# Kernel optimization log

Measured on AMD Instinct MI355X. Metric: run time of the kernel, lower is better.

## Reference

```python
import jax, jax.numpy as jnp
import numpy as np

B, D, NSEQ = 8, 512, 32
L0 = NSEQ * NSEQ          # 1024
H, DH = 8, 64             # n_head, d_head; H*DH == D
DFF = 2048
NLAYER = 2
EPS = 1e-6
SCALE = 1.0 / (DH ** 0.5)


def setup_inputs() -> dict:
    key = jax.random.key(0)
    ks = jax.random.split(key, 16)
    s = lambda fan: 1.0 / np.sqrt(fan)
    return {
        "embed1": jax.random.normal(ks[0], (B, D, L0), jnp.float32),
        "embed2": jax.random.normal(ks[1], (B, D, L0), jnp.float32),
        "cls_token": jax.random.normal(ks[2], (1, 1, D), jnp.float32),
        "Wq": jax.random.normal(ks[3], (NLAYER, D, D), jnp.float32) * s(D),
        "bq": jnp.zeros((NLAYER, D), jnp.float32),
        "Wk": jax.random.normal(ks[4], (NLAYER, D, D), jnp.float32) * s(D),
        "bk": jnp.zeros((NLAYER, D), jnp.float32),
        "Wv": jax.random.normal(ks[5], (NLAYER, D, D), jnp.float32) * s(D),
        "bv": jnp.zeros((NLAYER, D), jnp.float32),
        "Wo": jax.random.normal(ks[6], (NLAYER, D, D), jnp.float32) * s(D),
        "bo": jnp.zeros((NLAYER, D), jnp.float32),
        "ln1_g": jnp.ones((NLAYER, D), jnp.float32),
        "ln1_b": jnp.zeros((NLAYER, D), jnp.float32),
        "W1": jax.random.normal(ks[7], (NLAYER, DFF, D), jnp.float32) * s(D),
        "b1": jnp.zeros((NLAYER, DFF), jnp.float32),
        "W2": jax.random.normal(ks[8], (NLAYER, D, DFF), jnp.float32) * s(DFF),
        "b2": jnp.zeros((NLAYER, D), jnp.float32),
        "ln2_g": jnp.ones((NLAYER, D), jnp.float32),
        "ln2_b": jnp.zeros((NLAYER, D), jnp.float32),
    }


def _ln(x, g, b):
    m = jnp.mean(x, axis=-1, keepdims=True)
    v = jnp.mean(jnp.square(x - m), axis=-1, keepdims=True)
    return (x - m) * jax.lax.rsqrt(v + EPS) * g + b


def reference(embed1, embed2, cls_token, Wq, bq, Wk, bk, Wv, bv, Wo, bo,
              ln1_g, ln1_b, W1, b1, W2, b2, ln2_g, ln2_b):
    b = embed1.shape[0]
    cls = jnp.broadcast_to(cls_token, (b, 1, D))
    # [B, L0, D] with prepended cls -> [B, L, D]
    x1 = jnp.concatenate([cls, jnp.transpose(embed1, (0, 2, 1))], axis=1)
    x2 = jnp.concatenate([cls, jnp.transpose(embed2, (0, 2, 1))], axis=1)
    # mask_inputs is all ones vs i_pad=0 -> attn_mask all False (no masking)
    x = x1
    for l in range(NLAYER):
        q = (x  @ Wq[l].T + bq[l]).reshape(b, -1, H, DH)   # [B,L,H,DH]
        k = (x2 @ Wk[l].T + bk[l]).reshape(b, -1, H, DH)
        v = (x2 @ Wv[l].T + bv[l]).reshape(b, -1, H, DH)
        scores = jnp.einsum('bqhd,bkhd->bhqk', q, k) * SCALE
        attn = jax.nn.softmax(scores, axis=-1)
        ctx = jnp.einsum('bhqk,bkhd->bqhd', attn, v).reshape(b, -1, H * DH)
        att_out = ctx @ Wo[l].T + bo[l]
        x = _ln(x + att_out, ln1_g[l], ln1_b[l])
        h = jax.nn.gelu(x @ W1[l].T + b1[l], approximate=False)
        ffn = h @ W2[l].T + b2[l]
        x = _ln(x + ffn, ln2_g[l], ln2_b[l])
    return x
```

## Files before the change

kernel.cpp:

```cpp
#include <hip/hip_runtime.h>
#include <hip/hip_bf16.h>

constexpr int B_   = 8;
constexpr int D_   = 512;
constexpr int L0_  = 1024;
constexpr int L_   = 1025;
constexpr int H_   = 8;
constexpr int DH_  = 64;
constexpr int DFF_ = 2048;
constexpr int NLAYER_ = 2;
constexpr int M_   = B_ * L_;
constexpr int LP_  = 1088;
constexpr int NQT_ = 9;
constexpr int NSPLIT_ = 2;
constexpr float EPS_   = 1e-6f;
constexpr float SCALE_ = 0.125f;

#define DEV_INLINE __device__ __forceinline__

typedef __attribute__((ext_vector_type(8))) __bf16 bf16x8;
typedef __attribute__((ext_vector_type(4))) __bf16 bf16x4;
typedef __attribute__((ext_vector_type(4))) float  f32x4;
typedef __attribute__((ext_vector_type(4))) unsigned int u32x4;

union U4 { uint32_t u[4]; bf16x8 f; };

DEV_INLINE float gelu_exact(float x) {
    return 0.5f * x * (1.f + erff(x * 0.70710678118654752f));
}

DEV_INLINE uint16_t bfbits(float v) {
    __bf16 h = (__bf16)v;
    return __builtin_bit_cast(uint16_t, h);
}
DEV_INLINE uint32_t pk2f(float a, float b) {
    return (uint32_t)bfbits(a) | ((uint32_t)bfbits(b) << 16);
}
DEV_INLINE float bf2f(uint32_t bits16) {
    uint32_t u = bits16 << 16;
    return __builtin_bit_cast(float, u);
}

__global__ __launch_bounds__(256) void tobf16_kernel(
    const float* __restrict__ src, __bf16* __restrict__ dst, int n4) {
    int i = blockIdx.x * 256 + threadIdx.x;
    if (i >= n4) return;
    float4 v = *(const float4*)&src[i * 4];
    bf16x4 h;
    h[0] = (__bf16)v.x; h[1] = (__bf16)v.y;
    h[2] = (__bf16)v.z; h[3] = (__bf16)v.w;
    *(bf16x4*)&dst[i * 4] = h;
}

__global__ __launch_bounds__(256) void zero_vt_pad_kernel(__bf16* __restrict__ Vt) {
    constexpr int PAD = LP_ - L_;
    int idx = blockIdx.x * 256 + threadIdx.x;
    int total = B_ * H_ * DH_ * PAD;
    if (idx >= total) return;
    int row = idx / PAD;
    int c   = idx - row * PAD;
    Vt[(size_t)row * LP_ + L_ + c] = (__bf16)0.f;
}

__global__ __launch_bounds__(256) void write_cls_kernel(
    const float* __restrict__ cls, float* __restrict__ X1, float* __restrict__ X2) {
    int idx = blockIdx.x * 256 + threadIdx.x;
    int b = idx >> 9;
    int d = idx & 511;
    float v = cls[d];
    X1[(size_t)b * L_ * D_ + d] = v;
    X2[(size_t)b * L_ * D_ + d] = v;
}

__global__ __launch_bounds__(256) void transpose_embed_kernel(
    const float* __restrict__ e, float* __restrict__ X) {
    __shared__ float tile[32][33];
    int b  = blockIdx.z;
    int i0 = blockIdx.x * 32;
    int d0 = blockIdx.y * 32;
    int tx = threadIdx.x;
    int ty = threadIdx.y;
#pragma unroll
    for (int j = 0; j < 32; j += 8)
        tile[ty + j][tx] = e[((size_t)b * D_ + d0 + ty + j) * L0_ + i0 + tx];
    __syncthreads();
#pragma unroll
    for (int j = 0; j < 32; j += 8)
        X[((size_t)b * L_ + 1 + i0 + ty + j) * D_ + d0 + tx] = tile[tx][ty + j];
}

template <bool GELU, int OUTMODE>
__global__ __launch_bounds__(256) void gemm_mfma_kernel(
    const __bf16* __restrict__ A, const __bf16* __restrict__ Wh,
    const float* __restrict__ bias, float* __restrict__ C,
    __bf16* __restrict__ Ch, int M, int N, int K, float oscale) {
    constexpr int BM = 128, BN = 64, BK = 64;
    constexpr int LDK = BK + 8;
    __shared__ alignas(16) __bf16 Ahs[BM][LDK];
    __shared__ alignas(16) __bf16 Bhs[BN][LDK];

    const int GM = (M + BM - 1) / BM;
    const int nwg = gridDim.x;
    int bid = blockIdx.x;
    {
        int q = nwg >> 3, r = nwg & 7;
        int xcd = bid & 7, pos = bid >> 3;
        bid = (xcd < r) ? xcd * (q + 1) + pos
                        : r * (q + 1) + (xcd - r) * q + pos;
    }
    const int bn = bid / GM;
    const int bm = bid % GM;
    const int m0 = bm * BM;
    const int n0 = bn * BN;

    const int tid  = threadIdx.x;
    const int lane = tid & 63;
    const int wv   = tid >> 6;
    const int wr   = wv >> 1;
    const int wc   = wv & 1;
    const int fr   = lane & 15;
    const int fq   = lane >> 4;
    const int fq8  = fq * 8;
    const int mb   = wr * 64;
    const int nb   = wc * 32;

    const int srow = tid >> 2;
    const int scol = (tid & 3) * 16;
    size_t aOff[2];
#pragma unroll
    for (int rep = 0; rep < 2; ++rep) {
        int r = m0 + srow + rep * 64;
        if (r > M - 1) r = M - 1;
        aOff[rep] = (size_t)r * K + scol;
    }
    const size_t wOff = (size_t)(n0 + srow) * K + scol;

    f32x4 acc[4][2];
#pragma unroll
    for (int i = 0; i < 4; ++i)
#pragma unroll
        for (int j = 0; j < 2; ++j) acc[i][j] = (f32x4){0.f, 0.f, 0.f, 0.f};

    const int nk = K / BK;
    u32x4 aR[2][2], wR[2];
#pragma unroll
    for (int rep = 0; rep < 2; ++rep) {
        aR[rep][0] = *(const u32x4*)&A[aOff[rep]];
        aR[rep][1] = *(const u32x4*)&A[aOff[rep] + 8];
    }
    wR[0] = *(const u32x4*)&Wh[wOff];
    wR[1] = *(const u32x4*)&Wh[wOff + 8];

    for (int kt = 0; kt < nk; ++kt) {
#pragma unroll
        for (int rep = 0; rep < 2; ++rep) {
            *(u32x4*)&Ahs[srow + rep * 64][scol]     = aR[rep][0];
            *(u32x4*)&Ahs[srow + rep * 64][scol + 8] = aR[rep][1];
        }
        *(u32x4*)&Bhs[srow][scol]     = wR[0];
        *(u32x4*)&Bhs[srow][scol + 8] = wR[1];
        __syncthreads();

        if (kt + 1 < nk) {
            int k0 = (kt + 1) * BK;
#pragma unroll
            for (int rep = 0; rep < 2; ++rep) {
                aR[rep][0] = *(const u32x4*)&A[aOff[rep] + k0];
                aR[rep][1] = *(const u32x4*)&A[aOff[rep] + k0 + 8];
            }
            wR[0] = *(const u32x4*)&Wh[wOff + k0];
            wR[1] = *(const u32x4*)&Wh[wOff + k0 + 8];
        }

#pragma unroll
        for (int ks = 0; ks < 2; ++ks) {
            bf16x8 ah[4], bh[2];
#pragma unroll
            for (int i = 0; i < 4; ++i)
                ah[i] = *(bf16x8*)&Ahs[mb + i * 16 + fr][ks * 32 + fq8];
#pragma unroll
            for (int j = 0; j < 2; ++j)
                bh[j] = *(bf16x8*)&Bhs[nb + j * 16 + fr][ks * 32 + fq8];
#pragma unroll
            for (int i = 0; i < 4; ++i)
#pragma unroll
                for (int j = 0; j < 2; ++j)
                    acc[i][j] = __builtin_amdgcn_mfma_f32_16x16x32_bf16(ah[i], bh[j], acc[i][j], 0, 0, 0);
        }
        __syncthreads();
    }

    const int ccol0 = n0 + nb + fr;
    const float b0 = bias[ccol0];
    const float b1 = bias[ccol0 + 16];
#pragma unroll
    for (int i = 0; i < 4; ++i) {
#pragma unroll
        for (int r = 0; r < 4; ++r) {
            int row = m0 + mb + i * 16 + fq * 4 + r;
            if (row < M) {
                float v0 = acc[i][0][r] + b0;
                float v1 = acc[i][1][r] + b1;
                if (GELU) { v0 = gelu_exact(v0); v1 = gelu_exact(v1); }
                v0 *= oscale;
                v1 *= oscale;
                if (OUTMODE == 2) {
                    Ch[(size_t)row * N + ccol0]      = (__bf16)v0;
                    Ch[(size_t)row * N + ccol0 + 16] = (__bf16)v1;
                } else {
                    C[(size_t)row * N + ccol0]      = v0;
                    C[(size_t)row * N + ccol0 + 16] = v1;
                }
            }
        }
    }
}

__global__ __launch_bounds__(256) void gemm_kv_kernel(
    const __bf16* __restrict__ A, const __bf16* __restrict__ Wh,
    const float* __restrict__ biasK, const float* __restrict__ biasV,
    __bf16* __restrict__ Kb, __bf16* __restrict__ Vt) {
    constexpr int BM = 128, BN = 64, BK = 64, K = 512;
    constexpr int LDK = BK + 8;
    __shared__ alignas(16) __bf16 Ahs[BM][LDK];
    __shared__ alignas(16) __bf16 Bhs[BN][LDK];

    const int GM = (M_ + BM - 1) / BM;
    const int nwg = gridDim.x;
    int bid = blockIdx.x;
    {
        int q = nwg >> 3, r = nwg & 7;
        int xcd = bid & 7, pos = bid >> 3;
        bid = (xcd < r) ? xcd * (q + 1) + pos
                        : r * (q + 1) + (xcd - r) * q + pos;
    }
    const int bn = bid / GM;
    const int bm = bid % GM;
    const int m0 = bm * BM;
    const int n0 = bn * BN;

    const int tid  = threadIdx.x;
    const int lane = tid & 63;
    const int wv   = tid >> 6;
    const int wr   = wv >> 1;
    const int wc   = wv & 1;
    const int fr   = lane & 15;
    const int fq   = lane >> 4;
    const int fq8  = fq * 8;
    const int mb   = wr * 64;
    const int nb   = wc * 32;

    const int srow = tid >> 2;
    const int scol = (tid & 3) * 16;
    size_t aOff[2];
#pragma unroll
    for (int rep = 0; rep < 2; ++rep) {
        int r = m0 + srow + rep * 64;
        if (r > M_ - 1) r = M_ - 1;
        aOff[rep] = (size_t)r * K + scol;
    }
    const size_t wOff = (size_t)(n0 + srow) * K + scol;

    f32x4 acc[4][2];
#pragma unroll
    for (int i = 0; i < 4; ++i)
#pragma unroll
        for (int j = 0; j < 2; ++j) acc[i][j] = (f32x4){0.f, 0.f, 0.f, 0.f};

    const int nk = K / BK;
    u32x4 aR[2][2], wR[2];
#pragma unroll
    for (int rep = 0; rep < 2; ++rep) {
        aR[rep][0] = *(const u32x4*)&A[aOff[rep]];
        aR[rep][1] = *(const u32x4*)&A[aOff[rep] + 8];
    }
    wR[0] = *(const u32x4*)&Wh[wOff];
    wR[1] = *(const u32x4*)&Wh[wOff + 8];

    for (int kt = 0; kt < nk; ++kt) {
#pragma unroll
        for (int rep = 0; rep < 2; ++rep) {
            *(u32x4*)&Ahs[srow + rep * 64][scol]     = aR[rep][0];
            *(u32x4*)&Ahs[srow + rep * 64][scol + 8] = aR[rep][1];
        }
        *(u32x4*)&Bhs[srow][scol]     = wR[0];
        *(u32x4*)&Bhs[srow][scol + 8] = wR[1];
        __syncthreads();

        if (kt + 1 < nk) {
            int k0 = (kt + 1) * BK;
#pragma unroll
            for (int rep = 0; rep < 2; ++rep) {
                aR[rep][0] = *(const u32x4*)&A[aOff[rep] + k0];
                aR[rep][1] = *(const u32x4*)&A[aOff[rep] + k0 + 8];
            }
            wR[0] = *(const u32x4*)&Wh[wOff + k0];
            wR[1] = *(const u32x4*)&Wh[wOff + k0 + 8];
        }

#pragma unroll
        for (int ks = 0; ks < 2; ++ks) {
            bf16x8 ah[4], bh[2];
#pragma unroll
            for (int i = 0; i < 4; ++i)
                ah[i] = *(bf16x8*)&Ahs[mb + i * 16 + fr][ks * 32 + fq8];
#pragma unroll
            for (int j = 0; j < 2; ++j)
                bh[j] = *(bf16x8*)&Bhs[nb + j * 16 + fr][ks * 32 + fq8];
#pragma unroll
            for (int i = 0; i < 4; ++i)
#pragma unroll
                for (int j = 0; j < 2; ++j)
                    acc[i][j] = __builtin_amdgcn_mfma_f32_16x16x32_bf16(ah[i], bh[j], acc[i][j], 0, 0, 0);
        }
        __syncthreads();
    }

    const int ccol0 = n0 + nb + fr;
    if (n0 < 512) {
        const float b0 = biasK[ccol0];
        const float b1 = biasK[ccol0 + 16];
#pragma unroll
        for (int i = 0; i < 4; ++i) {
#pragma unroll
            for (int r = 0; r < 4; ++r) {
                int row = m0 + mb + i * 16 + fq * 4 + r;
                if (row < M_) {
                    Kb[(size_t)row * 512 + ccol0]      = (__bf16)(acc[i][0][r] + b0);
                    Kb[(size_t)row * 512 + ccol0 + 16] = (__bf16)(acc[i][1][r] + b1);
                }
            }
        }
    } else {
        const int cv = ccol0 - 512;
        const int h2 = cv >> 6, d2 = cv & 63;
        const float b0 = biasV[cv];
        const float b1 = biasV[cv + 16];
#pragma unroll
        for (int i = 0; i < 4; ++i) {
#pragma unroll
            for (int r = 0; r < 4; ++r) {
                int row = m0 + mb + i * 16 + fq * 4 + r;
                if (row < M_) {
                    int b2 = row / L_;
                    int l2 = row - b2 * L_;
                    size_t vb = (size_t)(b2 * H_ + h2) * DH_ * LP_;
                    Vt[vb + (size_t)d2 * LP_ + l2]        = (__bf16)(acc[i][0][r] + b0);
                    Vt[vb + (size_t)(d2 + 16) * LP_ + l2] = (__bf16)(acc[i][1][r] + b1);
                }
            }
        }
    }
}

__global__ __launch_bounds__(256) void attn_mfma_kernel(
    const __bf16* __restrict__ Qb, const __bf16* __restrict__ Kb,
    const __bf16* __restrict__ Vtb, __bf16* __restrict__ Opart,
    float* __restrict__ ml) {
    constexpr int LDP = 72;
    constexpr int NT = (L_ + 63) / 64;
    __shared__ alignas(16) __bf16 Kls[64][LDP];
    __shared__ alignas(16) __bf16 Vls[64][LDP];

    const int tid  = threadIdx.x;
    const int lane = tid & 63;
    const int wv   = tid >> 6;
    const int fr   = lane & 15;
    const int fq   = lane >> 4;
    const int fq8  = fq * 8;

    int bid = blockIdx.x;
    int swz = (bid & 7) * (NSPLIT_ * NQT_ * H_ * B_ / 8) + (bid >> 3);
    const int s   = swz / (NQT_ * H_ * B_);
    int rem = swz - s * (NQT_ * H_ * B_);
    const int qt = rem % NQT_;
    const int bh = rem / NQT_;
    const int h = bh & 7, b = bh >> 3;
    const int q0 = qt * 128 + wv * 32;
    const int T0 = (NT * s) / NSPLIT_;
    const int T1 = (NT * (s + 1)) / NSPLIT_;
    const size_t obase = (size_t)b * L_ * D_ + h * DH_;

    bf16x8 bqh[2][2];
#pragma unroll
    for (int g = 0; g < 2; ++g) {
        int gq = q0 + 16 * g + fr; if (gq > L_ - 1) gq = L_ - 1;
        const __bf16* qrow = Qb + (size_t)(b * L_ + gq) * D_ + h * DH_;
#pragma unroll
        for (int ss = 0; ss < 2; ++ss)
            bqh[g][ss] = *(const bf16x8*)&qrow[ss * 32 + fq8];
    }

    float m[2] = {-1e30f, -1e30f};
    float lsum[2] = {0.f, 0.f};
    f32x4 oA[2][4];
#pragma unroll
    for (int g = 0; g < 2; ++g)
#pragma unroll
        for (int c = 0; c < 4; ++c) oA[g][c] = (f32x4){0.f, 0.f, 0.f, 0.f};

    const int sr  = tid >> 2;
    const int scb = (tid & 3) * 8;
    const size_t kRowBase = (size_t)(b * L_) * D_ + h * DH_ + scb;
    const size_t vRowBase = ((size_t)bh * DH_ + sr) * LP_ + scb;

    u32x4 kR[2], vR[2];
    {
        int gr = T0 * 64 + sr; if (gr > L_ - 1) gr = L_ - 1;
        const __bf16* kp = Kb + kRowBase + (size_t)gr * D_;
        const __bf16* vp = Vtb + vRowBase + T0 * 64;
        kR[0] = *(const u32x4*)&kp[0];  kR[1] = *(const u32x4*)&kp[32];
        vR[0] = *(const u32x4*)&vp[0];  vR[1] = *(const u32x4*)&vp[32];
        *(u32x4*)&Kls[sr][scb]      = kR[0];
        *(u32x4*)&Kls[sr][scb + 32] = kR[1];
        *(u32x4*)&Vls[sr][scb]      = vR[0];
        *(u32x4*)&Vls[sr][scb + 32] = vR[1];
    }

    for (int t = T0; t < T1; ++t) {
        const int kt = t * 64;
        __syncthreads();

        if (t + 1 < T1) {
            int gr = kt + 64 + sr; if (gr > L_ - 1) gr = L_ - 1;
            const __bf16* kp = Kb + kRowBase + (size_t)gr * D_;
            const __bf16* vp = Vtb + vRowBase + (kt + 64);
            kR[0] = *(const u32x4*)&kp[0];  kR[1] = *(const u32x4*)&kp[32];
            vR[0] = *(const u32x4*)&vp[0];  vR[1] = *(const u32x4*)&vp[32];
        }

        const bool fullTile = (kt + 64 <= L_);
        float p0[4][4], p1[4][4];
#pragma unroll
        for (int c = 0; c < 4; ++c) {
            const int row = 16 * c + fr;
            bf16x8 ah0 = *(bf16x8*)&Kls[row][fq8];
            bf16x8 ah1 = *(bf16x8*)&Kls[row][32 + fq8];
#pragma unroll
            for (int g = 0; g < 2; ++g) {
                f32x4 sacc = (f32x4){0.f, 0.f, 0.f, 0.f};
                sacc = __builtin_amdgcn_mfma_f32_16x16x32_bf16(ah0, bqh[g][0], sacc, 0, 0, 0);
                sacc = __builtin_amdgcn_mfma_f32_16x16x32_bf16(ah1, bqh[g][1], sacc, 0, 0, 0);
                if (fullTile) {
#pragma unroll
                    for (int rr = 0; rr < 4; ++rr) {
                        if (g == 0) p0[c][rr] = sacc[rr]; else p1[c][rr] = sacc[rr];
                    }
                } else {
#pragma unroll
                    for (int rr = 0; rr < 4; ++rr) {
                        int k = kt + 16 * c + 4 * fq + rr;
                        float val = (k < L_) ? sacc[rr] : -1e30f;
                        if (g == 0) p0[c][rr] = val; else p1[c][rr] = val;
                    }
                }
            }
        }

        bf16x8 pah[2][2];
#pragma unroll
        for (int g = 0; g < 2; ++g) {
            float (*p)[4] = (g == 0) ? p0 : p1;
            float t0 = p[0][0];
#pragma unroll
            for (int c = 0; c < 4; ++c)
#pragma unroll
                for (int rr = 0; rr < 4; ++rr) t0 = fmaxf(t0, p[c][rr]);
            t0 = fmaxf(t0, __shfl_xor(t0, 16));
            t0 = fmaxf(t0, __shfl_xor(t0, 32));
            float mn = fmaxf(m[g], t0);
            const bool noresc = __all(mn == m[g]);
            float sclq = noresc ? 1.f : __expf(m[g] - mn);
            m[g] = mn;
            float ls = 0.f;
#pragma unroll
            for (int c = 0; c < 4; ++c)
#pragma unroll
                for (int rr = 0; rr < 4; ++rr) {
                    float e = __expf(p[c][rr] - mn);
                    p[c][rr] = e;
                    ls += e;
                }
            ls += __shfl_xor(ls, 16);
            ls += __shfl_xor(ls, 32);
            lsum[g] = lsum[g] * sclq + ls;
            if (!noresc) {
#pragma unroll
                for (int rr = 0; rr < 4; ++rr) {
                    float sO = __shfl(sclq, 4 * fq + rr);
#pragma unroll
                    for (int c2 = 0; c2 < 4; ++c2) oA[g][c2][rr] *= sO;
                }
            }

            uint32_t pqh[4][2];
#pragma unroll
            for (int c = 0; c < 4; ++c) {
                pqh[c][0] = pk2f(p[c][0], p[c][1]);
                pqh[c][1] = pk2f(p[c][2], p[c][3]);
            }
            const int src0 = fr + ((fq & 1) << 5);
            const int src1 = src0 + 16;
            const bool sel = (fq >> 1) != 0;
#pragma unroll
            for (int ss = 0; ss < 2; ++ss) {
                const int c0 = 2 * ss, c1 = 2 * ss + 1;
                uint32_t A0 = (uint32_t)__shfl((int)pqh[c0][0], src0);
                uint32_t A1 = (uint32_t)__shfl((int)pqh[c0][1], src0);
                uint32_t A2 = (uint32_t)__shfl((int)pqh[c0][0], src1);
                uint32_t A3 = (uint32_t)__shfl((int)pqh[c0][1], src1);
                uint32_t B0 = (uint32_t)__shfl((int)pqh[c1][0], src0);
                uint32_t B1 = (uint32_t)__shfl((int)pqh[c1][1], src0);
                uint32_t B2 = (uint32_t)__shfl((int)pqh[c1][0], src1);
                uint32_t B3 = (uint32_t)__shfl((int)pqh[c1][1], src1);
                U4 uh;
                uh.u[0] = sel ? B0 : A0; uh.u[1] = sel ? B1 : A1;
                uh.u[2] = sel ? B2 : A2; uh.u[3] = sel ? B3 : A3;
                pah[g][ss] = uh.f;
            }
        }

#pragma unroll
        for (int c2 = 0; c2 < 4; ++c2) {
            const int row = 16 * c2 + fr;
            bf16x8 vh0 = *(bf16x8*)&Vls[row][fq8];
            bf16x8 vh1 = *(bf16x8*)&Vls[row][32 + fq8];
#pragma unroll
            for (int g = 0; g < 2; ++g) {
                f32x4 o = oA[g][c2];
                o = __builtin_amdgcn_mfma_f32_16x16x32_bf16(pah[g][0], vh0, o, 0, 0, 0);
                o = __builtin_amdgcn_mfma_f32_16x16x32_bf16(pah[g][1], vh1, o, 0, 0, 0);
                oA[g][c2] = o;
            }
        }

        __syncthreads();
        if (t + 1 < T1) {
            *(u32x4*)&Kls[sr][scb]      = kR[0];
            *(u32x4*)&Kls[sr][scb + 32] = kR[1];
            *(u32x4*)&Vls[sr][scb]      = vR[0];
            *(u32x4*)&Vls[sr][scb + 32] = vR[1];
        }
    }

    __bf16* Op = Opart + (size_t)s * M_ * D_;
#pragma unroll
    for (int g = 0; g < 2; ++g) {
#pragma unroll
        for (int rr = 0; rr < 4; ++rr) {
            int row = q0 + 16 * g + 4 * fq + rr;
            if (row < L_) {
#pragma unroll
                for (int c2 = 0; c2 < 4; ++c2)
                    Op[obase + (size_t)row * D_ + 16 * c2 + fr] = (__bf16)oA[g][c2][rr];
            }
        }
        if (fq == 0) {
            int qrow = q0 + 16 * g + fr;
            if (qrow < L_) {
                size_t mlidx = (((size_t)s * B_ + b) * H_ + h) * L_ + qrow;
                ml[mlidx * 2]     = m[g];
                ml[mlidx * 2 + 1] = lsum[g];
            }
        }
    }
}

__global__ __launch_bounds__(256) void attn_merge_kernel(
    const __bf16* __restrict__ Opart, const float* __restrict__ ml,
    __bf16* __restrict__ Out) {
    int idx = blockIdx.x * 256 + threadIdx.x;
    if (idx >= M_ * 64) return;
    int row = idx >> 6;
    int seg = idx & 63;
    int col0 = seg * 8;
    int h = col0 >> 6;
    int b = row / L_;
    int l = row - b * L_;
    float ms[NSPLIT_], ls[NSPLIT_];
    float mm = -1e30f;
#pragma unroll
    for (int s = 0; s < NSPLIT_; ++s) {
        size_t mi = ((((size_t)s * B_ + b) * H_ + h) * L_ + l) * 2;
        ms[s] = ml[mi];
        ls[s] = ml[mi + 1];
        mm = fmaxf(mm, ms[s]);
    }
    float wsum = 0.f, w[NSPLIT_];
#pragma unroll
    for (int s = 0; s < NSPLIT_; ++s) {
        w[s] = __expf(ms[s] - mm);
        wsum += w[s] * ls[s];
    }
    float inv = 1.f / wsum;
#pragma unroll
    for (int s = 0; s < NSPLIT_; ++s) w[s] *= inv;

    size_t base = (size_t)row * D_ + col0;
    float o[8] = {0.f, 0.f, 0.f, 0.f, 0.f, 0.f, 0.f, 0.f};
#pragma unroll
    for (int s = 0; s < NSPLIT_; ++s) {
        const __bf16* Os = Opart + (size_t)s * M_ * D_;
        u32x4 a = *(const u32x4*)&Os[base];
#pragma unroll
        for (int i = 0; i < 4; ++i) {
            o[2 * i]     += w[s] * bf2f(a[i] & 0xffffu);
            o[2 * i + 1] += w[s] * bf2f(a[i] >> 16);
        }
    }
    U4 u;
#pragma unroll
    for (int i = 0; i < 4; ++i)
        u.u[i] = pk2f(o[2 * i], o[2 * i + 1]);
    *(u32x4*)&Out[base] = *(u32x4*)&u.u[0];
}

template <bool HIOUT>
__global__ __launch_bounds__(256) void add_ln_kernel(
    const float* __restrict__ X, const float* __restrict__ Y,
    const float* __restrict__ g, const float* __restrict__ be,
    float* __restrict__ Out, __bf16* __restrict__ Oh) {
    int wave = threadIdx.x >> 6;
    int lane = threadIdx.x & 63;
    int row = blockIdx.x * 4 + wave;
    if (row >= M_) return;
    size_t base = (size_t)row * D_;
    int c0 = lane * 4, c1 = 256 + lane * 4;
    float4 xa = *(const float4*)&X[base + c0];
    float4 xb = *(const float4*)&X[base + c1];
    float4 ya = *(const float4*)&Y[base + c0];
    float4 yb = *(const float4*)&Y[base + c1];
    float v[8] = {xa.x + ya.x, xa.y + ya.y, xa.z + ya.z, xa.w + ya.w,
                  xb.x + yb.x, xb.y + yb.y, xb.z + yb.z, xb.w + yb.w};
    float s = 0.f, s2 = 0.f;
#pragma unroll
    for (int i = 0; i < 8; ++i) { s += v[i]; s2 = fmaf(v[i], v[i], s2); }
#pragma unroll
    for (int off = 32; off > 0; off >>= 1) {
        s  += __shfl_xor(s, off);
        s2 += __shfl_xor(s2, off);
    }
    float mean = s * (1.f / D_);
    float var  = s2 * (1.f / D_) - mean * mean;
    float rstd = rsqrtf(var + EPS_);
    float4 ga = *(const float4*)&g[c0];
    float4 gb = *(const float4*)&g[c1];
    float4 ba = *(const float4*)&be[c0];
    float4 bb = *(const float4*)&be[c1];
    float o[8];
    o[0] = (v[0] - mean) * rstd * ga.x + ba.x;
    o[1] = (v[1] - mean) * rstd * ga.y + ba.y;
    o[2] = (v[2] - mean) * rstd * ga.z + ba.z;
    o[3] = (v[3] - mean) * rstd * ga.w + ba.w;
    o[4] = (v[4] - mean) * rstd * gb.x + bb.x;
    o[5] = (v[5] - mean) * rstd * gb.y + bb.y;
    o[6] = (v[6] - mean) * rstd * gb.z + bb.z;
    o[7] = (v[7] - mean) * rstd * gb.w + bb.w;
    *(float4*)&Out[base + c0] = make_float4(o[0], o[1], o[2], o[3]);
    *(float4*)&Out[base + c1] = make_float4(o[4], o[5], o[6], o[7]);
    if (HIOUT) {
        bf16x4 h0, h1;
#pragma unroll
        for (int i = 0; i < 4; ++i) {
            h0[i] = (__bf16)o[i];
            h1[i] = (__bf16)o[4 + i];
        }
        *(bf16x4*)&Oh[base + c0] = h0;
        *(bf16x4*)&Oh[base + c1] = h1;
    }
}

extern "C" void kernel_launch(void* const* d_in, const int* in_sizes, int n_in,
                              void* d_out, int out_size, void* d_ws, size_t ws_size,
                              hipStream_t stream) {
    const float* embed1 = (const float*)d_in[0];
    const float* embed2 = (const float*)d_in[1];
    const float* cls    = (const float*)d_in[2];
    const float* Wq = (const float*)d_in[3];
    const float* bq = (const float*)d_in[4];
    const float* Wk = (const float*)d_in[5];
    const float* bk = (const float*)d_in[6];
    const float* Wv = (const float*)d_in[7];
    const float* bv = (const float*)d_in[8];
    const float* Wo = (const float*)d_in[9];
    const float* bo = (const float*)d_in[10];
    const float* ln1g = (const float*)d_in[11];
    const float* ln1b = (const float*)d_in[12];
    const float* W1 = (const float*)d_in[13];
    const float* b1 = (const float*)d_in[14];
    const float* W2 = (const float*)d_in[15];
    const float* b2 = (const float*)d_in[16];
    const float* ln2g = (const float*)d_in[17];
    const float* ln2b = (const float*)d_in[18];

    const size_t SZ = (size_t)M_ * D_;
    float* ws = (float*)d_ws;
    float* X   = ws;
    __bf16* Xh = (__bf16*)(ws + SZ);
    __bf16* X2h = (__bf16*)(ws + SZ + SZ / 2);
    float* Tb  = ws + 2 * SZ;
    __bf16* Tbh = (__bf16*)(ws + 2 * SZ + SZ / 2);
    __bf16* Qbh = (__bf16*)(ws + 3 * SZ);
    float* WoOut  = (float*)(ws + 3 * SZ);
    __bf16* Kbh = (__bf16*)(ws + 4 * SZ);
    __bf16* Vtb = (__bf16*)(ws + 5 * SZ);
    __bf16* Hbh = (__bf16*)(ws + 5 * SZ);
    float* mlBuf   = ws + 6 * SZ + SZ / 2;
    __bf16* Opart  = (__bf16*)(ws + 7 * SZ);
    __bf16* wreg = (__bf16*)(ws + 9 * SZ);

    const size_t NQl = (size_t)D_ * D_;
    const size_t NQ  = (size_t)NLAYER_ * NQl;
    const size_t NF  = (size_t)NLAYER_ * DFF_ * D_;
    __bf16* Wqh  = wreg;
    __bf16* Wkvh = Wqh + NQ;
    __bf16* Woh  = Wkvh + 2 * NQ;
    __bf16* W1h  = Woh + NQ;
    __bf16* W2h  = W1h + NF;

    tobf16_kernel<<<(int)(NQ / 4 + 255) / 256, 256, 0, stream>>>(Wq, Wqh, (int)(NQ / 4));
    tobf16_kernel<<<(int)(NQ / 4 + 255) / 256, 256, 0, stream>>>(Wo, Woh, (int)(NQ / 4));
    tobf16_kernel<<<(int)(NF / 4 + 255) / 256, 256, 0, stream>>>(W1, W1h, (int)(NF / 4));
    tobf16_kernel<<<(int)(NF / 4 + 255) / 256, 256, 0, stream>>>(W2, W2h, (int)(NF / 4));
    for (int l = 0; l < NLAYER_; ++l) {
        tobf16_kernel<<<(int)(NQl / 4 + 255) / 256, 256, 0, stream>>>(
            Wk + l * NQl, Wkvh + l * 2 * NQl, (int)(NQl / 4));
        tobf16_kernel<<<(int)(NQl / 4 + 255) / 256, 256, 0, stream>>>(
            Wv + l * NQl, Wkvh + l * 2 * NQl + NQl, (int)(NQl / 4));
    }

    float* X2tmp = Tb;
    write_cls_kernel<<<(B_ * D_) / 256, 256, 0, stream>>>(cls, X, X2tmp);
    transpose_embed_kernel<<<dim3(L0_ / 32, D_ / 32, B_), dim3(32, 8), 0, stream>>>(embed1, X);
    transpose_embed_kernel<<<dim3(L0_ / 32, D_ / 32, B_), dim3(32, 8), 0, stream>>>(embed2, X2tmp);
    tobf16_kernel<<<(int)(SZ / 4 + 255) / 256, 256, 0, stream>>>(X, Xh, (int)(SZ / 4));
    tobf16_kernel<<<(int)(SZ / 4 + 255) / 256, 256, 0, stream>>>(X2tmp, X2h, (int)(SZ / 4));

    const int GM = (M_ + 127) / 128;
    const int g512  = GM * (512 / 64);
    const int g1024 = GM * (1024 / 64);
    const int g2048 = GM * (2048 / 64);
    const int gpad  = (B_ * H_ * DH_ * (LP_ - L_) + 255) / 256;
    const int gmerge = (M_ * 64 + 255) / 256;

    for (int l = 0; l < NLAYER_; ++l) {
        const size_t oQ = (size_t)l * NQl;
        const size_t oF = (size_t)l * DFF_ * D_;

        gemm_mfma_kernel<false, 2><<<g512, 256, 0, stream>>>(
            Xh, Wqh + oQ, bq + l * D_, nullptr, Qbh, M_, D_, D_, SCALE_);
        gemm_kv_kernel<<<g1024, 256, 0, stream>>>(
            X2h, Wkvh + l * 2 * NQl, bk + l * D_, bv + l * D_, Kbh, Vtb);
        zero_vt_pad_kernel<<<gpad, 256, 0, stream>>>(Vtb);

        attn_mfma_kernel<<<NSPLIT_ * NQT_ * H_ * B_, 256, 0, stream>>>(
            Qbh, Kbh, Vtb, Opart, mlBuf);
        attn_merge_kernel<<<gmerge, 256, 0, stream>>>(Opart, mlBuf, Tbh);

        gemm_mfma_kernel<false, 0><<<g512, 256, 0, stream>>>(
            Tbh, Woh + oQ, bo + l * D_, WoOut, nullptr, M_, D_, D_, 1.f);

        add_ln_kernel<true><<<(M_ + 3) / 4, 256, 0, stream>>>(
            X, WoOut, ln1g + l * D_, ln1b + l * D_, X, Xh);

        gemm_mfma_kernel<true, 2><<<g2048, 256, 0, stream>>>(
            Xh, W1h + oF, b1 + l * DFF_, nullptr, Hbh, M_, DFF_, D_, 1.f);
        gemm_mfma_kernel<false, 0><<<g512, 256, 0, stream>>>(
            Hbh, W2h + oF, b2 + l * D_, Tb, nullptr, M_, D_, DFF_, 1.f);

        if (l == NLAYER_ - 1) {
            add_ln_kernel<false><<<(M_ + 3) / 4, 256, 0, stream>>>(
                X, Tb, ln2g + l * D_, ln2b + l * D_, (float*)d_out, nullptr);
        } else {
            add_ln_kernel<true><<<(M_ + 3) / 4, 256, 0, stream>>>(
                X, Tb, ln2g + l * D_, ln2b + l * D_, X, Xh);
        }
    }
}
```

Measured before the change: 554.9 us.

## Rewrite attention inner loop with 32x32x16 MFMA and transposed layout

The attention kernel now uses 32x32x16 bf16 MFMA instead of 16x16x32, computing S^T and O^T so each lane owns one query row. Softmax row statistics then need only a single cross-half shuffle. The P operand is rebuilt with two xor shuffles instead of many indexed shuffles, and output stores become vectorized per row. The aim is fewer shuffles, fewer LDS reads and fewer MFMA issues per tile. In exchange each lane holds larger accumulator registers, which may affect occupancy.

```diff
diff --git a/kernel.cpp b/kernel.cpp
--- a/kernel.cpp
+++ b/kernel.cpp
@@ -18,10 +18,11 @@
 
 #define DEV_INLINE __device__ __forceinline__
 
-typedef __attribute__((ext_vector_type(8))) __bf16 bf16x8;
-typedef __attribute__((ext_vector_type(4))) __bf16 bf16x4;
-typedef __attribute__((ext_vector_type(4))) float  f32x4;
-typedef __attribute__((ext_vector_type(4))) unsigned int u32x4;
+typedef __attribute__((ext_vector_type(8)))  __bf16 bf16x8;
+typedef __attribute__((ext_vector_type(4)))  __bf16 bf16x4;
+typedef __attribute__((ext_vector_type(4)))  float  f32x4;
+typedef __attribute__((ext_vector_type(16))) float  f32x16;
+typedef __attribute__((ext_vector_type(4)))  unsigned int u32x4;
 
 union U4 { uint32_t u[4]; bf16x8 f; };
 
@@ -365,9 +366,8 @@
     const int tid  = threadIdx.x;
     const int lane = tid & 63;
     const int wv   = tid >> 6;
-    const int fr   = lane & 15;
-    const int fq   = lane >> 4;
-    const int fq8  = fq * 8;
+    const int la   = lane & 31;
+    const int hl   = lane >> 5;
 
     int bid = blockIdx.x;
     int swz = (bid & 7) * (NSPLIT_ * NQT_ * H_ * B_ / 8) + (bid >> 3);
@@ -381,23 +381,19 @@
     const int T1 = (NT * (s + 1)) / NSPLIT_;
     const size_t obase = (size_t)b * L_ * D_ + h * DH_;
 
-    bf16x8 bqh[2][2];
-#pragma unroll
-    for (int g = 0; g < 2; ++g) {
-        int gq = q0 + 16 * g + fr; if (gq > L_ - 1) gq = L_ - 1;
+    bf16x8 bq[4];
+    {
+        int gq = q0 + la; if (gq > L_ - 1) gq = L_ - 1;
         const __bf16* qrow = Qb + (size_t)(b * L_ + gq) * D_ + h * DH_;
 #pragma unroll
-        for (int ss = 0; ss < 2; ++ss)
-            bqh[g][ss] = *(const bf16x8*)&qrow[ss * 32 + fq8];
-    }
-
-    float m[2] = {-1e30f, -1e30f};
-    float lsum[2] = {0.f, 0.f};
-    f32x4 oA[2][4];
-#pragma unroll
-    for (int g = 0; g < 2; ++g)
-#pragma unroll
-        for (int c = 0; c < 4; ++c) oA[g][c] = (f32x4){0.f, 0.f, 0.f, 0.f};
+        for (int c = 0; c < 4; ++c)
+            bq[c] = *(const bf16x8*)&qrow[c * 16 + hl * 8];
+    }
+
+    float m = -1e30f, lsum = 0.f;
+    f32x16 oT0, oT1;
+#pragma unroll
+    for (int r = 0; r < 16; ++r) { oT0[r] = 0.f; oT1[r] = 0.f; }
 
     const int sr  = tid >> 2;
     const int scb = (tid & 3) * 8;
@@ -430,107 +426,76 @@
         }
 
         const bool fullTile = (kt + 64 <= L_);
-        float p0[4][4], p1[4][4];
-#pragma unroll
-        for (int c = 0; c < 4; ++c) {
-            const int row = 16 * c + fr;
-            bf16x8 ah0 = *(bf16x8*)&Kls[row][fq8];
-            bf16x8 ah1 = *(bf16x8*)&Kls[row][32 + fq8];
-#pragma unroll
-            for (int g = 0; g < 2; ++g) {
-                f32x4 sacc = (f32x4){0.f, 0.f, 0.f, 0.f};
-                sacc = __builtin_amdgcn_mfma_f32_16x16x32_bf16(ah0, bqh[g][0], sacc, 0, 0, 0);
-                sacc = __builtin_amdgcn_mfma_f32_16x16x32_bf16(ah1, bqh[g][1], sacc, 0, 0, 0);
-                if (fullTile) {
-#pragma unroll
-                    for (int rr = 0; rr < 4; ++rr) {
-                        if (g == 0) p0[c][rr] = sacc[rr]; else p1[c][rr] = sacc[rr];
-                    }
-                } else {
-#pragma unroll
-                    for (int rr = 0; rr < 4; ++rr) {
-                        int k = kt + 16 * c + 4 * fq + rr;
-                        float val = (k < L_) ? sacc[rr] : -1e30f;
-                        if (g == 0) p0[c][rr] = val; else p1[c][rr] = val;
-                    }
+#pragma unroll
+        for (int st = 0; st < 2; ++st) {
+            const int ko = st * 32;
+
+            f32x16 sacc;
+#pragma unroll
+            for (int r = 0; r < 16; ++r) sacc[r] = 0.f;
+#pragma unroll
+            for (int c = 0; c < 4; ++c) {
+                bf16x8 ak = *(bf16x8*)&Kls[ko + la][c * 16 + hl * 8];
+                sacc = __builtin_amdgcn_mfma_f32_32x32x16_bf16(ak, bq[c], sacc, 0, 0, 0);
+            }
+
+            float p[16];
+            if (fullTile) {
+#pragma unroll
+                for (int r = 0; r < 16; ++r) p[r] = sacc[r];
+            } else {
+#pragma unroll
+                for (int r = 0; r < 16; ++r) {
+                    int kg = kt + ko + (r & 3) + 8 * (r >> 2) + 4 * hl;
+                    p[r] = (kg < L_) ? sacc[r] : -1e30f;
                 }
             }
-        }
-
-        bf16x8 pah[2][2];
-#pragma unroll
-        for (int g = 0; g < 2; ++g) {
-            float (*p)[4] = (g == 0) ? p0 : p1;
-            float t0 = p[0][0];
-#pragma unroll
-            for (int c = 0; c < 4; ++c)
-#pragma unroll
-                for (int rr = 0; rr < 4; ++rr) t0 = fmaxf(t0, p[c][rr]);
-            t0 = fmaxf(t0, __shfl_xor(t0, 16));
+
+            float t0 = p[0];
+#pragma unroll
+            for (int r = 1; r < 16; ++r) t0 = fmaxf(t0, p[r]);
             t0 = fmaxf(t0, __shfl_xor(t0, 32));
-            float mn = fmaxf(m[g], t0);
-            const bool noresc = __all(mn == m[g]);
-            float sclq = noresc ? 1.f : __expf(m[g] - mn);
-            m[g] = mn;
+            float mn = fmaxf(m, t0);
+            const bool noresc = __all(mn == m);
+            float sclq = noresc ? 1.f : __expf(m - mn);
+            m = mn;
             float ls = 0.f;
 #pragma unroll
-            for (int c = 0; c < 4; ++c)
-#pragma unroll
-                for (int rr = 0; rr < 4; ++rr) {
-                    float e = __expf(p[c][rr] - mn);
-                    p[c][rr] = e;
-                    ls += e;
-                }
-            ls += __shfl_xor(ls, 16);
+            for (int r = 0; r < 16; ++r) {
+                float e = __expf(p[r] - mn);
+                p[r] = e;
+                ls += e;
+            }
             ls += __shfl_xor(ls, 32);
-            lsum[g] = lsum[g] * sclq + ls;
+            lsum = lsum * sclq + ls;
             if (!noresc) {
 #pragma unroll
-                for (int rr = 0; rr < 4; ++rr) {
-                    float sO = __shfl(sclq, 4 * fq + rr);
-#pragma unroll
-                    for (int c2 = 0; c2 < 4; ++c2) oA[g][c2][rr] *= sO;
-                }
-            }
-
-            uint32_t pqh[4][2];
-#pragma unroll
-            for (int c = 0; c < 4; ++c) {
-                pqh[c][0] = pk2f(p[c][0], p[c][1]);
-                pqh[c][1] = pk2f(p[c][2], p[c][3]);
-            }
-            const int src0 = fr + ((fq & 1) << 5);
-            const int src1 = src0 + 16;
-            const bool sel = (fq >> 1) != 0;
-#pragma unroll
-            for (int ss = 0; ss < 2; ++ss) {
-                const int c0 = 2 * ss, c1 = 2 * ss + 1;
-                uint32_t A0 = (uint32_t)__shfl((int)pqh[c0][0], src0);
-                uint32_t A1 = (uint32_t)__shfl((int)pqh[c0][1], src0);
-                uint32_t A2 = (uint32_t)__shfl((int)pqh[c0][0], src1);
-                uint32_t A3 = (uint32_t)__shfl((int)pqh[c0][1], src1);
-                uint32_t B0 = (uint32_t)__shfl((int)pqh[c1][0], src0);
-                uint32_t B1 = (uint32_t)__shfl((int)pqh[c1][1], src0);
-                uint32_t B2 = (uint32_t)__shfl((int)pqh[c1][0], src1);
-                uint32_t B3 = (uint32_t)__shfl((int)pqh[c1][1], src1);
+                for (int r = 0; r < 16; ++r) { oT0[r] *= sclq; oT1[r] *= sclq; }
+            }
+
+            bf16x8 pb[2];
+#pragma unroll
+            for (int cc = 0; cc < 2; ++cc) {
+                uint32_t G0 = pk2f(p[8 * cc + 0], p[8 * cc + 1]);
+                uint32_t G1 = pk2f(p[8 * cc + 2], p[8 * cc + 3]);
+                uint32_t G2 = pk2f(p[8 * cc + 4], p[8 * cc + 5]);
+                uint32_t G3 = pk2f(p[8 * cc + 6], p[8 * cc + 7]);
+                uint32_t x0 = (uint32_t)__shfl_xor((int)(hl ? G0 : G2), 32);
+                uint32_t x1 = (uint32_t)__shfl_xor((int)(hl ? G1 : G3), 32);
                 U4 uh;
-                uh.u[0] = sel ? B0 : A0; uh.u[1] = sel ? B1 : A1;
-                uh.u[2] = sel ? B2 : A2; uh.u[3] = sel ? B3 : A3;
-                pah[g][ss] = uh.f;
-            }
-        }
-
-#pragma unroll
-        for (int c2 = 0; c2 < 4; ++c2) {
-            const int row = 16 * c2 + fr;
-            bf16x8 vh0 = *(bf16x8*)&Vls[row][fq8];
-            bf16x8 vh1 = *(bf16x8*)&Vls[row][32 + fq8];
-#pragma unroll
-            for (int g = 0; g < 2; ++g) {
-                f32x4 o = oA[g][c2];
-                o = __builtin_amdgcn_mfma_f32_16x16x32_bf16(pah[g][0], vh0, o, 0, 0, 0);
-                o = __builtin_amdgcn_mfma_f32_16x16x32_bf16(pah[g][1], vh1, o, 0, 0, 0);
-                oA[g][c2] = o;
+                uh.u[0] = hl ? x0 : G0;
+                uh.u[1] = hl ? x1 : G1;
+                uh.u[2] = hl ? G2 : x0;
+                uh.u[3] = hl ? G3 : x1;
+                pb[cc] = uh.f;
+            }
+
+#pragma unroll
+            for (int cc = 0; cc < 2; ++cc) {
+                bf16x8 av0 = *(bf16x8*)&Vls[la][ko + cc * 16 + hl * 8];
+                bf16x8 av1 = *(bf16x8*)&Vls[32 + la][ko + cc * 16 + hl * 8];
+                oT0 = __builtin_amdgcn_mfma_f32_32x32x16_bf16(av0, pb[cc], oT0, 0, 0, 0);
+                oT1 = __builtin_amdgcn_mfma_f32_32x32x16_bf16(av1, pb[cc], oT1, 0, 0, 0);
             }
         }
 
@@ -544,24 +509,23 @@
     }
 
     __bf16* Op = Opart + (size_t)s * M_ * D_;
-#pragma unroll
-    for (int g = 0; g < 2; ++g) {
-#pragma unroll
-        for (int rr = 0; rr < 4; ++rr) {
-            int row = q0 + 16 * g + 4 * fq + rr;
-            if (row < L_) {
-#pragma unroll
-                for (int c2 = 0; c2 < 4; ++c2)
-                    Op[obase + (size_t)row * D_ + 16 * c2 + fr] = (__bf16)oA[g][c2][rr];
-            }
-        }
-        if (fq == 0) {
-            int qrow = q0 + 16 * g + fr;
-            if (qrow < L_) {
-                size_t mlidx = (((size_t)s * B_ + b) * H_ + h) * L_ + qrow;
-                ml[mlidx * 2]     = m[g];
-                ml[mlidx * 2 + 1] = lsum[g];
-            }
+    int qrow = q0 + la;
+    if (qrow < L_) {
+        __bf16* orow = Op + obase + (size_t)qrow * D_;
+#pragma unroll
+        for (int bb = 0; bb < 4; ++bb) {
+            uint2 uu0, uu1;
+            uu0.x = pk2f(oT0[4 * bb + 0], oT0[4 * bb + 1]);
+            uu0.y = pk2f(oT0[4 * bb + 2], oT0[4 * bb + 3]);
+            uu1.x = pk2f(oT1[4 * bb + 0], oT1[4 * bb + 1]);
+            uu1.y = pk2f(oT1[4 * bb + 2], oT1[4 * bb + 3]);
+            *(uint2*)&orow[bb * 8 + hl * 4]      = uu0;
+            *(uint2*)&orow[32 + bb * 8 + hl * 4] = uu1;
+        }
+        if (hl == 0) {
+            size_t mlidx = (((size_t)s * B_ + b) * H_ + h) * L_ + qrow;
+            ml[mlidx * 2]     = m;
+            ml[mlidx * 2 + 1] = lsum;
         }
     }
 }
```

New measurement: 523.7 us. -5.6%, faster.
